# Kernel tuning notes

Measured on AMD Instinct MI355X. Metric: run time of the kernel, lower is better.

Reference implementation:

```python
import jax, jax.numpy as jnp
import numpy as np

B, T, D, H = 4096, 16, 512, 8
DH = D // H
EPS = 1e-5

def _layer_norm(x, w, b):
    mu = jnp.mean(x, axis=-1, keepdims=True)
    var = jnp.mean(jnp.square(x - mu), axis=-1, keepdims=True)
    return (x - mu) * jax.lax.rsqrt(var + EPS) * w + b

def setup_inputs() -> dict:
    key = jax.random.key(0)
    ks = jax.random.split(key, 12)
    inp = {
        'structural_output': jax.random.normal(ks[0], (B, T, D), jnp.float32),
        'position_embedding_clustering_coefficient': jax.random.normal(ks[1], (B, T, D), jnp.float32),
        'position_embedding_bidirectional_links_ratio': jax.random.normal(ks[2], (B, T, D), jnp.float32),
        'exist_nodes': jax.random.randint(ks[3], (B, T), 0, 2, jnp.int32),
        'pos_emb': jax.random.normal(ks[4], (T, D), jnp.float32) * 0.02,
        'Qw': jax.random.normal(ks[5], (D, D), jnp.float32) / np.sqrt(D),
        'Kw': jax.random.normal(ks[6], (D, D), jnp.float32) / np.sqrt(D),
        'Vw': jax.random.normal(ks[7], (D, D), jnp.float32) / np.sqrt(D),
        'ln_w': jnp.ones((D,), jnp.float32),
        'ln_b': jnp.zeros((D,), jnp.float32),
        'ff1_w': jax.random.normal(ks[8], (D, D), jnp.float32) / np.sqrt(D),
        'ff1_b': jnp.zeros((D,), jnp.float32),
        'prelu_a': jnp.array(0.25, jnp.float32),
        'ff2_w': jax.random.normal(ks[9], (2, D), jnp.float32) / np.sqrt(D),
        'ff2_b': jnp.zeros((2,), jnp.float32),
    }
    return inp

def reference(structural_output, position_embedding_clustering_coefficient,
              position_embedding_bidirectional_links_ratio, exist_nodes,
              pos_emb, Qw, Kw, Vw, ln_w, ln_b, ff1_w, ff1_b, prelu_a, ff2_w, ff2_b):
    x = structural_output
    # temporal input = x + positional embeddings, then shared LayerNorm
    t_in = _layer_norm(
        x + pos_emb[None, :, :]
        + position_embedding_clustering_coefficient
        + position_embedding_bidirectional_links_ratio,
        ln_w, ln_b)
    # fused-style QKV projections, split into heads [B,T,H,DH]
    q = (t_in @ Qw).reshape(B, T, H, DH)
    k = (t_in @ Kw).reshape(B, T, H, DH)
    v = (t_in @ Vw).reshape(B, T, H, DH)
    scores = jnp.einsum('bihd,bjhd->bhij', q, k) / np.sqrt(DH)  # [B,H,T,T]
    causal = jnp.tril(jnp.ones((T, T), bool))
    scores = jnp.where(causal[None, None], scores, jnp.float32(-1e9))
    attn = jax.nn.softmax(scores, axis=-1)  # dropout is identity at inference
    out = jnp.einsum('bhij,bjhd->bihd', attn, v).reshape(B, T, D)
    # residual with pre-norm input, shared LayerNorm again
    y = _layer_norm(out + x, ln_w, ln_b)
    # feed forward: Linear(D,D) -> PReLU -> Linear(D,2)
    h = y @ ff1_w.T + ff1_b
    h = jnp.maximum(h, 0) + prelu_a * jnp.minimum(h, 0)
    return h @ ff2_w.T + ff2_b
```

## Files before the change

kernel.cpp:

```cpp
#include <hip/hip_runtime.h>

#define NROWS 65536
#define DD 512
#define EPS_LN 1e-5f

typedef __bf16 bfx8 __attribute__((ext_vector_type(8)));
typedef float fx4 __attribute__((ext_vector_type(4)));

__device__ __forceinline__ unsigned short f2bf(float f) {
  unsigned int u = __builtin_bit_cast(unsigned int, f);
  u += 0x7fffu + ((u >> 16) & 1u);
  return (unsigned short)(u >> 16);
}
__device__ __forceinline__ float bflo(unsigned int u) { return __builtin_bit_cast(float, u << 16); }
__device__ __forceinline__ float bfhi(unsigned int u) { return __builtin_bit_cast(float, u & 0xffff0000u); }
__device__ __forceinline__ unsigned int pack2(float a, float b) {
  return (unsigned int)f2bf(a) | ((unsigned int)f2bf(b) << 16);
}
__device__ __forceinline__ float wave_sum(float v) {
  #pragma unroll
  for (int off = 32; off; off >>= 1) v += __shfl_xor(v, off);
  return v;
}
__device__ __forceinline__ void glds16(const unsigned short* g, unsigned short* l) {
  __builtin_amdgcn_global_load_lds(
      (const __attribute__((address_space(1))) unsigned int*)g,
      (__attribute__((address_space(3))) unsigned int*)l, 16, 0, 0);
}

__global__ __launch_bounds__(256) void prep_weights(
    const float* __restrict__ Qw, const float* __restrict__ Kw, const float* __restrict__ Vw,
    const float* __restrict__ ff1w,
    unsigned short* __restrict__ WqkvT, unsigned short* __restrict__ W1T) {
  int idx = blockIdx.x * 256 + threadIdx.x;
  if (idx < 1536 * 512) {
    int j = idx >> 9, k = idx & 511;
    const float* src = (j < 512) ? Qw : (j < 1024 ? Kw : Vw);
    WqkvT[idx] = f2bf(src[k * 512 + (j & 511)]);
  } else {
    int i2 = idx - 1536 * 512;
    W1T[i2] = f2bf(ff1w[i2]);
  }
}

__global__ __launch_bounds__(256) void ln1_kernel(
    const float* __restrict__ x, const float* __restrict__ pcc, const float* __restrict__ pblr,
    const float* __restrict__ pos, const float* __restrict__ lnw, const float* __restrict__ lnb,
    unsigned short* __restrict__ t_in) {
  int row = blockIdx.x * 4 + (threadIdx.x >> 6);
  int lane = threadIdx.x & 63;
  size_t base = (size_t)row * DD + lane * 8;
  int t = row & 15;
  const fx4* x4 = (const fx4*)(x + base);
  const fx4* p4 = (const fx4*)(pcc + base);
  const fx4* q4 = (const fx4*)(pblr + base);
  const fx4* e4 = (const fx4*)(pos + t * DD + lane * 8);
  fx4 a0 = x4[0], a1 = x4[1], b0 = p4[0], b1 = p4[1], c0 = q4[0], c1 = q4[1], d0 = e4[0], d1 = e4[1];
  float s[8];
  #pragma unroll
  for (int j = 0; j < 4; ++j) { s[j] = a0[j] + b0[j] + c0[j] + d0[j]; s[j+4] = a1[j] + b1[j] + c1[j] + d1[j]; }
  float sum = 0.f;
  #pragma unroll
  for (int j = 0; j < 8; ++j) sum += s[j];
  sum = wave_sum(sum);
  float mu = sum * (1.0f / 512.0f);
  float vs = 0.f;
  #pragma unroll
  for (int j = 0; j < 8; ++j) { float d = s[j] - mu; vs += d * d; }
  vs = wave_sum(vs);
  float rs = rsqrtf(vs * (1.0f / 512.0f) + EPS_LN);
  const fx4* w4 = (const fx4*)(lnw + lane * 8);
  const fx4* bb4 = (const fx4*)(lnb + lane * 8);
  fx4 w0 = w4[0], w1 = w4[1], g0 = bb4[0], g1 = bb4[1];
  float o[8];
  #pragma unroll
  for (int j = 0; j < 4; ++j) { o[j] = (s[j] - mu) * rs * w0[j] + g0[j]; o[j+4] = (s[j+4] - mu) * rs * w1[j] + g1[j]; }
  uint4 pk;
  pk.x = pack2(o[0], o[1]); pk.y = pack2(o[2], o[3]); pk.z = pack2(o[4], o[5]); pk.w = pack2(o[6], o[7]);
  *(uint4*)(t_in + base) = pk;
}

template<int NT, bool EPI>
__global__ __launch_bounds__(256) void gemm_bt(
    const unsigned short* __restrict__ A, const unsigned short* __restrict__ BT,
    unsigned short* __restrict__ C, int ldc,
    const float* __restrict__ bias, const float* __restrict__ prelu_a) {
  __shared__ unsigned short As[128 * 64];
  __shared__ unsigned short Bs[128 * 64];
  int tid = threadIdx.x;
  int nwg = gridDim.x;
  int bid = blockIdx.x;
  int cpx = nwg >> 3;
  int swz = (bid & 7) * cpx + (bid >> 3);
  int col0 = (swz % NT) * 128, row0 = (swz / NT) * 128;
  int wid = tid >> 6, lane = tid & 63;
  int wm = (wid >> 1) * 64, wn = (wid & 1) * 64;
  int srow = (lane >> 3);
  int skk = (((lane & 7) ^ srow) & 7) * 8;
  fx4 acc[4][4] = {};
  for (int k0 = 0; k0 < 512; k0 += 64) {
    #pragma unroll
    for (int c = 0; c < 4; ++c) {
      int chunk = wid * 4 + c;
      int r = chunk * 8 + srow;
      glds16(A + (size_t)(row0 + r) * 512 + k0 + skk, As + chunk * 512);
      glds16(BT + (size_t)(col0 + r) * 512 + k0 + skk, Bs + chunk * 512);
    }
    __syncthreads();
    #pragma unroll
    for (int ks = 0; ks < 2; ++ks) {
      int soff = ((ks * 4 + (lane >> 4)) ^ (lane & 7)) * 8;
      bfx8 af[4], bfr[4];
      #pragma unroll
      for (int m = 0; m < 4; ++m) af[m] = *(const bfx8*)(As + (wm + m * 16 + (lane & 15)) * 64 + soff);
      #pragma unroll
      for (int n = 0; n < 4; ++n) bfr[n] = *(const bfx8*)(Bs + (wn + n * 16 + (lane & 15)) * 64 + soff);
      #pragma unroll
      for (int m = 0; m < 4; ++m)
        #pragma unroll
        for (int n = 0; n < 4; ++n)
          acc[m][n] = __builtin_amdgcn_mfma_f32_16x16x32_bf16(af[m], bfr[n], acc[m][n], 0, 0, 0);
    }
    __syncthreads();
  }
  int fq = lane >> 4, fr = lane & 15;
  float pa = EPI ? *prelu_a : 0.f;
  #pragma unroll
  for (int m = 0; m < 4; ++m) {
    #pragma unroll
    for (int n = 0; n < 4; ++n) {
      int rbase = row0 + wm + m * 16 + fq * 4;
      int cidx = col0 + wn + n * 16 + fr;
      float bv = EPI ? bias[cidx] : 0.f;
      #pragma unroll
      for (int r = 0; r < 4; ++r) {
        float v = acc[m][n][r];
        if constexpr (EPI) { v += bv; v = fmaxf(v, 0.f) + pa * fminf(v, 0.f); }
        C[(size_t)(rbase + r) * ldc + cidx] = f2bf(v);
      }
    }
  }
}

__global__ __launch_bounds__(256) void attn_ln2_kernel(
    const unsigned short* __restrict__ qkv, const float* __restrict__ x,
    const float* __restrict__ lnw, const float* __restrict__ lnb,
    unsigned short* __restrict__ y) {
  __shared__ unsigned short q_s[16 * 520];
  __shared__ unsigned short k_s[16 * 520];
  __shared__ unsigned short v_s[16 * 520];
  __shared__ float p_s[8 * 16 * 18];
  int b = blockIdx.x, tid = threadIdx.x;
  #pragma unroll
  for (int c = 0; c < 12; ++c) {
    int v = c * 256 + tid;
    int i = v / 192, colv = v % 192, col = colv * 8;
    uint4 d = *(const uint4*)(qkv + (size_t)(b * 16 + i) * 1536 + col);
    unsigned short* dst = (col < 512) ? (q_s + i * 520 + col)
                        : (col < 1024) ? (k_s + i * 520 + (col - 512))
                                       : (v_s + i * 520 + (col - 1024));
    *(uint4*)dst = d;
  }
  __syncthreads();
  if (tid < 128) {
    int h = tid >> 4, i = tid & 15;
    uint4 qv[8];
    #pragma unroll
    for (int db = 0; db < 8; ++db) qv[db] = *(const uint4*)(q_s + i * 520 + h * 64 + db * 8);
    float sc[16];
    float mx = -3e38f;
    #pragma unroll
    for (int j = 0; j < 16; ++j) {
      float acc = 0.f;
      const unsigned short* kr = k_s + j * 520 + h * 64;
      #pragma unroll
      for (int db = 0; db < 8; ++db) {
        uint4 kv = *(const uint4*)(kr + db * 8);
        acc += bflo(qv[db].x) * bflo(kv.x) + bfhi(qv[db].x) * bfhi(kv.x);
        acc += bflo(qv[db].y) * bflo(kv.y) + bfhi(qv[db].y) * bfhi(kv.y);
        acc += bflo(qv[db].z) * bflo(kv.z) + bfhi(qv[db].z) * bfhi(kv.z);
        acc += bflo(qv[db].w) * bflo(kv.w) + bfhi(qv[db].w) * bfhi(kv.w);
      }
      acc = (j <= i) ? acc * 0.125f : -3e38f;
      sc[j] = acc;
      mx = fmaxf(mx, acc);
    }
    float sum = 0.f;
    #pragma unroll
    for (int j = 0; j < 16; ++j) {
      float e = (j <= i) ? __expf(sc[j] - mx) : 0.f;
      sc[j] = e; sum += e;
    }
    float inv = 1.0f / sum;
    float* prow = p_s + (h * 16 + i) * 18;
    #pragma unroll
    for (int j = 0; j < 16; ++j) prow[j] = sc[j] * inv;
  }
  __syncthreads();
  int lane = tid & 63;
  #pragma unroll
  for (int rep = 0; rep < 4; ++rep) {
    int i = rep * 4 + (tid >> 6);
    int col = lane * 8, h = col >> 6;
    const float* prow = p_s + (h * 16 + i) * 18;
    float o[8] = {0, 0, 0, 0, 0, 0, 0, 0};
    #pragma unroll
    for (int j = 0; j < 16; ++j) {
      float p = prow[j];
      uint4 vv = *(const uint4*)(v_s + j * 520 + col);
      o[0] += p * bflo(vv.x); o[1] += p * bfhi(vv.x);
      o[2] += p * bflo(vv.y); o[3] += p * bfhi(vv.y);
      o[4] += p * bflo(vv.z); o[5] += p * bfhi(vv.z);
      o[6] += p * bflo(vv.w); o[7] += p * bfhi(vv.w);
    }
    size_t base = (size_t)(b * 16 + i) * 512 + col;
    const fx4* x4 = (const fx4*)(x + base);
    fx4 xa = x4[0], xb = x4[1];
    float s[8];
    #pragma unroll
    for (int j = 0; j < 4; ++j) { s[j] = o[j] + xa[j]; s[j+4] = o[j+4] + xb[j]; }
    float sum = 0.f;
    #pragma unroll
    for (int j = 0; j < 8; ++j) sum += s[j];
    sum = wave_sum(sum);
    float mu = sum * (1.0f / 512.0f);
    float vs = 0.f;
    #pragma unroll
    for (int j = 0; j < 8; ++j) { float d = s[j] - mu; vs += d * d; }
    vs = wave_sum(vs);
    float rs = rsqrtf(vs * (1.0f / 512.0f) + EPS_LN);
    const fx4* w4 = (const fx4*)(lnw + col);
    const fx4* bb4 = (const fx4*)(lnb + col);
    fx4 w0 = w4[0], w1 = w4[1], g0 = bb4[0], g1 = bb4[1];
    float oo[8];
    #pragma unroll
    for (int j = 0; j < 4; ++j) { oo[j] = (s[j] - mu) * rs * w0[j] + g0[j]; oo[j+4] = (s[j+4] - mu) * rs * w1[j] + g1[j]; }
    uint4 pk;
    pk.x = pack2(oo[0], oo[1]); pk.y = pack2(oo[2], oo[3]); pk.z = pack2(oo[4], oo[5]); pk.w = pack2(oo[6], oo[7]);
    *(uint4*)(y + base) = pk;
  }
}

__global__ __launch_bounds__(256) void ff2_kernel(
    const unsigned short* __restrict__ h, const float* __restrict__ w2,
    const float* __restrict__ b2, float* __restrict__ out) {
  int row = blockIdx.x * 4 + (threadIdx.x >> 6);
  int lane = threadIdx.x & 63;
  size_t base = (size_t)row * DD + lane * 8;
  uint4 hv = *(const uint4*)(h + base);
  float f[8];
  f[0] = bflo(hv.x); f[1] = bfhi(hv.x); f[2] = bflo(hv.y); f[3] = bfhi(hv.y);
  f[4] = bflo(hv.z); f[5] = bfhi(hv.z); f[6] = bflo(hv.w); f[7] = bfhi(hv.w);
  const fx4* w0p = (const fx4*)(w2 + lane * 8);
  const fx4* w1p = (const fx4*)(w2 + 512 + lane * 8);
  fx4 w00 = w0p[0], w01 = w0p[1], w10 = w1p[0], w11 = w1p[1];
  float a0 = 0.f, a1 = 0.f;
  #pragma unroll
  for (int j = 0; j < 4; ++j) {
    a0 += f[j] * w00[j] + f[j+4] * w01[j];
    a1 += f[j] * w10[j] + f[j+4] * w11[j];
  }
  a0 = wave_sum(a0);
  a1 = wave_sum(a1);
  if (lane == 0) {
    out[(size_t)row * 2 + 0] = a0 + b2[0];
    out[(size_t)row * 2 + 1] = a1 + b2[1];
  }
}

extern "C" void kernel_launch(void* const* d_in, const int* in_sizes, int n_in,
                              void* d_out, int out_size, void* d_ws, size_t ws_size,
                              hipStream_t stream) {
  const float* x    = (const float*)d_in[0];
  const float* pcc  = (const float*)d_in[1];
  const float* pblr = (const float*)d_in[2];
  const float* pos  = (const float*)d_in[4];
  const float* Qw   = (const float*)d_in[5];
  const float* Kw   = (const float*)d_in[6];
  const float* Vw   = (const float*)d_in[7];
  const float* lnw  = (const float*)d_in[8];
  const float* lnb  = (const float*)d_in[9];
  const float* ff1w = (const float*)d_in[10];
  const float* ff1b = (const float*)d_in[11];
  const float* pra  = (const float*)d_in[12];
  const float* ff2w = (const float*)d_in[13];
  const float* ff2b = (const float*)d_in[14];
  float* out = (float*)d_out;

  char* ws = (char*)d_ws;
  unsigned short* WqkvT = (unsigned short*)ws;
  unsigned short* W1T   = (unsigned short*)(ws + 1572864);
  unsigned short* t_in  = (unsigned short*)(ws + 2097152);
  unsigned short* qkv   = (unsigned short*)(ws + 2097152 + 67108864);
  unsigned short* ybuf  = qkv;
  unsigned short* hbuf  = t_in;

  prep_weights<<<4096, 256, 0, stream>>>(Qw, Kw, Vw, ff1w, WqkvT, W1T);
  ln1_kernel<<<NROWS / 4, 256, 0, stream>>>(x, pcc, pblr, pos, lnw, lnb, t_in);
  gemm_bt<12, false><<<12 * (NROWS / 128), 256, 0, stream>>>(
      t_in, WqkvT, qkv, 1536, nullptr, nullptr);
  attn_ln2_kernel<<<4096, 256, 0, stream>>>(qkv, x, lnw, lnb, ybuf);
  gemm_bt<4, true><<<4 * (NROWS / 128), 256, 0, stream>>>(
      ybuf, W1T, hbuf, 512, ff1b, pra);
  ff2_kernel<<<NROWS / 4, 256, 0, stream>>>(hbuf, ff2w, ff2b, out);
}
```

Before: 753.8 us.

## Compute attention scores with MFMA and load Q directly from global

The QK^T score computation in the attention+LN kernel moves from scalar bf16 dot products on half the threads to 16x16x32 bf16 MFMA instructions across all four waves. Each wave handles two heads and does the masked softmax with 16-lane shuffles. Q is read straight from global memory instead of being staged in LDS, and K is stored with an XOR-swizzled layout to avoid bank conflicts. The probability buffer gets a per-head offset for the same reason. This removes scalar FMA work and LDS traffic, at the cost of uncoalesced-ish direct Q loads and more index arithmetic.

```diff
diff --git a/kernel.cpp b/kernel.cpp
--- a/kernel.cpp
+++ b/kernel.cpp
@@ -146,63 +146,60 @@
     const unsigned short* __restrict__ qkv, const float* __restrict__ x,
     const float* __restrict__ lnw, const float* __restrict__ lnb,
     unsigned short* __restrict__ y) {
-  __shared__ unsigned short q_s[16 * 520];
-  __shared__ unsigned short k_s[16 * 520];
-  __shared__ unsigned short v_s[16 * 520];
-  __shared__ float p_s[8 * 16 * 18];
+  __shared__ __attribute__((aligned(16))) unsigned short k_s[16 * 576];
+  __shared__ __attribute__((aligned(16))) unsigned short v_s[16 * 520];
+  __shared__ float p_s[8 * 16 * 18 + 16];
   int b = blockIdx.x, tid = threadIdx.x;
   #pragma unroll
-  for (int c = 0; c < 12; ++c) {
+  for (int c = 0; c < 8; ++c) {
     int v = c * 256 + tid;
-    int i = v / 192, colv = v % 192, col = colv * 8;
-    uint4 d = *(const uint4*)(qkv + (size_t)(b * 16 + i) * 1536 + col);
-    unsigned short* dst = (col < 512) ? (q_s + i * 520 + col)
-                        : (col < 1024) ? (k_s + i * 520 + (col - 512))
-                                       : (v_s + i * 520 + (col - 1024));
-    *(uint4*)dst = d;
+    int i = v >> 7, colv = v & 127;
+    uint4 d = *(const uint4*)(qkv + (size_t)(b * 16 + i) * 1536 + 512 + colv * 8);
+    if (colv < 64) {
+      int ph = colv ^ (i & 7);
+      *(uint4*)(k_s + i * 576 + ph * 8) = d;
+    } else {
+      *(uint4*)(v_s + i * 520 + (colv - 64) * 8) = d;
+    }
   }
   __syncthreads();
-  if (tid < 128) {
-    int h = tid >> 4, i = tid & 15;
-    uint4 qv[8];
-    #pragma unroll
-    for (int db = 0; db < 8; ++db) qv[db] = *(const uint4*)(q_s + i * 520 + h * 64 + db * 8);
-    float sc[16];
-    float mx = -3e38f;
-    #pragma unroll
-    for (int j = 0; j < 16; ++j) {
-      float acc = 0.f;
-      const unsigned short* kr = k_s + j * 520 + h * 64;
-      #pragma unroll
-      for (int db = 0; db < 8; ++db) {
-        uint4 kv = *(const uint4*)(kr + db * 8);
-        acc += bflo(qv[db].x) * bflo(kv.x) + bfhi(qv[db].x) * bfhi(kv.x);
-        acc += bflo(qv[db].y) * bflo(kv.y) + bfhi(qv[db].y) * bfhi(kv.y);
-        acc += bflo(qv[db].z) * bflo(kv.z) + bfhi(qv[db].z) * bfhi(kv.z);
-        acc += bflo(qv[db].w) * bflo(kv.w) + bfhi(qv[db].w) * bfhi(kv.w);
+  {
+    int wv = tid >> 6, lane = tid & 63;
+    int g = lane >> 4, fr = lane & 15;
+    #pragma unroll
+    for (int hh = 0; hh < 2; ++hh) {
+      int h = wv * 2 + hh;
+      fx4 s = {};
+      #pragma unroll
+      for (int ks = 0; ks < 2; ++ks) {
+        bfx8 aq = *(const bfx8*)(qkv + (size_t)(b * 16 + fr) * 1536 + h * 64 + ks * 32 + g * 8);
+        int ch = (h * 8 + ks * 4 + g) ^ (fr & 7);
+        bfx8 bk = *(const bfx8*)(k_s + fr * 576 + ch * 8);
+        s = __builtin_amdgcn_mfma_f32_16x16x32_bf16(aq, bk, s, 0, 0, 0);
       }
-      acc = (j <= i) ? acc * 0.125f : -3e38f;
-      sc[j] = acc;
-      mx = fmaxf(mx, acc);
-    }
-    float sum = 0.f;
-    #pragma unroll
-    for (int j = 0; j < 16; ++j) {
-      float e = (j <= i) ? __expf(sc[j] - mx) : 0.f;
-      sc[j] = e; sum += e;
-    }
-    float inv = 1.0f / sum;
-    float* prow = p_s + (h * 16 + i) * 18;
-    #pragma unroll
-    for (int j = 0; j < 16; ++j) prow[j] = sc[j] * inv;
+      #pragma unroll
+      for (int r = 0; r < 4; ++r) {
+        int i = g * 4 + r;
+        bool keep = (fr <= i);
+        float sv = keep ? s[r] * 0.125f : -1e30f;
+        float m = sv;
+        #pragma unroll
+        for (int off = 1; off < 16; off <<= 1) m = fmaxf(m, __shfl_xor(m, off));
+        float e = keep ? __expf(sv - m) : 0.f;
+        float sum = e;
+        #pragma unroll
+        for (int off = 1; off < 16; off <<= 1) sum += __shfl_xor(sum, off);
+        p_s[(h * 16 + i) * 18 + h * 2 + fr] = e / sum;
+      }
+    }
   }
   __syncthreads();
   int lane = tid & 63;
   #pragma unroll
   for (int rep = 0; rep < 4; ++rep) {
     int i = rep * 4 + (tid >> 6);
-    int col = lane * 8, h = col >> 6;
-    const float* prow = p_s + (h * 16 + i) * 18;
+    int col = lane * 8, h = lane >> 3;
+    const float* prow = p_s + (h * 16 + i) * 18 + h * 2;
     float o[8] = {0, 0, 0, 0, 0, 0, 0, 0};
     #pragma unroll
     for (int j = 0; j < 16; ++j) {
```

After: 728.0 us. -3.4%, faster.
